# Kernel tuning notes

Measured on AMD Instinct MI355X. Metric: run time of the kernel, lower is better.

Reference implementation:

```python
import jax, jax.numpy as jnp
import numpy as np

B, T, HID = 2, 512, 1024
H, D, K = 16, 64, 4          # heads, head_dim, short-conv kernel
P = H * D                    # projection_dim
E, TOPK, I, IS = 8, 2, 768, 768  # experts, top_k, expert inter, shared inter
EPS = 1e-5


def setup_inputs() -> dict:
    key = jax.random.key(0)
    ks = jax.random.split(key, 24)
    def r(i, shape, s=0.02):
        return jax.random.normal(ks[i], shape, jnp.float32) * s
    return {
        "x": jax.random.normal(ks[0], (B, T, HID), jnp.float32),
        "norm1_w": jnp.ones((HID,), jnp.float32),
        "wq": r(1, (HID, P)), "wk": r(2, (HID, P)), "wv": r(3, (HID, P)),
        "cq": r(4, (P, K), 0.5), "ck": r(5, (P, K), 0.5), "cv": r(6, (P, K), 0.5),
        "fa": r(7, (HID, D)), "fb": r(8, (D, P)), "bp": r(9, (HID, H)),
        "ga": r(10, (HID, D)), "gb": r(11, (D, P)),
        "A_log": jnp.log(jax.random.uniform(ks[12], (H, 1), jnp.float32, 1.0, 16.0)),
        "dt_bias": r(13, (H, D), 0.1),
        "onorm_w": jnp.ones((D,), jnp.float32),
        "wo": r(14, (P, HID)),
        "norm2_w": jnp.ones((HID,), jnp.float32),
        "gate_w": r(15, (HID, E)), "gate_b": r(16, (E,), 0.1),
        "wg_e": r(17, (E, HID, I)), "wu_e": r(18, (E, HID, I)), "wd_e": r(19, (E, I, HID)),
        "wg_s": r(20, (HID, IS)), "wu_s": r(21, (HID, IS)), "wd_s": r(22, (IS, HID)),
    }


def _rms(x, w, eps=EPS):
    return x * jax.lax.rsqrt(jnp.mean(x * x, axis=-1, keepdims=True) + eps) * w


def _dwconv_silu(x, w):
    # causal depthwise conv, NLC layout: out[b,t,c] = sum_k w[c,k] * x[b, t-(K-1)+k, c]
    xp = jnp.pad(x, ((0, 0), (K - 1, 0), (0, 0)))
    out = sum(w[:, k] * xp[:, k:k + x.shape[1], :] for k in range(K))
    return jax.nn.silu(out)


def _delta_attn(x, wq, wk, wv, cq, ck, cv, fa, fb, bp, ga, gb, A_log, dt_bias, onorm_w, wo):
    q = _dwconv_silu(x @ wq, cq).reshape(B, T, H, D)
    k = _dwconv_silu(x @ wk, ck).reshape(B, T, H, D)
    v = _dwconv_silu(x @ wv, cv).reshape(B, T, H, D)
    # L2-style rms normalization of q/k (no weight, eps=1e-6), then asymmetric scaling
    q = q * jax.lax.rsqrt(jnp.mean(q * q, -1, keepdims=True) + 1e-6)
    k = k * jax.lax.rsqrt(jnp.mean(k * k, -1, keepdims=True) + 1e-6)
    scale = float(D) ** -0.5
    q = (scale ** 2) * q
    k = scale * k
    # fine-grained per-channel gated decay + per-head write strength
    a = ((x @ fa) @ fb).reshape(B, T, H, D)
    g = jnp.exp(-jnp.exp(A_log)[None, None] * jax.nn.softplus(a + dt_bias))  # (B,T,H,D)
    beta = jax.nn.sigmoid(x @ bp)  # (B,T,H)

    def step(S, qkvgb):
        qt, kt, vt, gt, bt = qkvgb            # (B,H,D) each, bt (B,H)
        S = S * gt[..., None]                  # decay over key dim, S: (B,H,Dk,Dv)
        pred = jnp.einsum('bhk,bhkv->bhv', kt, S)
        S = S + jnp.einsum('bhk,bhv->bhkv', kt, (vt - pred) * bt[..., None])
        o = jnp.einsum('bhk,bhkv->bhv', qt, S)
        return S, o

    xs = tuple(jnp.moveaxis(t_, 1, 0) for t_ in (q, k, v, g, beta))
    S0 = jnp.zeros((B, H, D, D), x.dtype)
    _, o = jax.lax.scan(step, S0, xs)
    o = jnp.moveaxis(o, 0, 1)                  # (B,T,H,D)
    gate = ((x @ ga) @ gb).reshape(B, T, H, D)
    o = _rms(o, onorm_w) * jax.nn.sigmoid(gate)
    return o.reshape(B, T, P) @ wo


def _moe(x, gate_w, gate_b, wg_e, wu_e, wd_e, wg_s, wu_s, wd_s):
    n = x.reshape(-1, HID)                     # (N, HID)
    scores = jax.nn.sigmoid(n @ gate_w)        # sigmoid router
    biased = scores + gate_b                   # e_score_correction bias (selection only)
    _, inds = jax.lax.top_k(biased, TOPK)      # n_group==1 -> plain top-k
    w = jnp.take_along_axis(scores, inds, -1)  # gather ORIGINAL scores
    w = w / (w.sum(-1, keepdims=True) + 1e-20) # renormalize; routed_scaling=1.0
    N = n.shape[0]
    comb = jnp.zeros((N, E), n.dtype).at[jnp.arange(N)[:, None], inds].add(w)
    hg = jnp.einsum('nd,edi->eni', n, wg_e)
    hu = jnp.einsum('nd,edi->eni', n, wu_e)
    eo = jnp.einsum('eni,eih->enh', jax.nn.silu(hg) * hu, wd_e)
    routed = jnp.einsum('ne,enh->nh', comb, eo)
    shared = (jax.nn.silu(n @ wg_s) * (n @ wu_s)) @ wd_s
    return (routed + shared).reshape(x.shape)


def _forward(x, norm1_w, wq, wk, wv, cq, ck, cv, fa, fb, bp, ga, gb, A_log, dt_bias,
             onorm_w, wo, norm2_w, gate_w, gate_b, wg_e, wu_e, wd_e, wg_s, wu_s, wd_s):
    h = x + _delta_attn(_rms(x, norm1_w), wq, wk, wv, cq, ck, cv, fa, fb, bp, ga, gb,
                        A_log, dt_bias, onorm_w, wo)
    return h + _moe(_rms(h, norm2_w), gate_w, gate_b, wg_e, wu_e, wd_e, wg_s, wu_s, wd_s)


def reference(x, norm1_w, wq, wk, wv, cq, ck, cv, fa, fb, bp, ga, gb, A_log, dt_bias,
              onorm_w, wo, norm2_w, gate_w, gate_b, wg_e, wu_e, wd_e, wg_s, wu_s, wd_s):
    return _forward(x, norm1_w, wq, wk, wv, cq, ck, cv, fa, fb, bp, ga, gb, A_log,
                    dt_bias, onorm_w, wo, norm2_w, gate_w, gate_b, wg_e, wu_e, wd_e,
                    wg_s, wu_s, wd_s)
```

## Files before the change

### kernel.cpp

```cpp
#include <hip/hip_runtime.h>
#include <hip/hip_bf16.h>
#include <math.h>

#define Bb 2
#define Tt 512
#define HIDD 1024
#define Hh 16
#define Dd 64
#define Pp 1024
#define Kc 4
#define Ee 8
#define Ii 768
#define ISs 768
#define Ntok (Bb*Tt)
#define NASSIGN (2*Ntok)
#define NPAD 2112
#define CH 16
#define NCH (Tt/CH)

typedef __attribute__((ext_vector_type(8))) short bf16x8;
typedef __attribute__((ext_vector_type(4))) float floatx4;

__device__ __forceinline__ float sigmoidf_(float x){ return 1.f/(1.f+expf(-x)); }
__device__ __forceinline__ float siluf_(float x){ return x/(1.f+expf(-x)); }
__device__ __forceinline__ float bf2f(__hip_bfloat16 b){ return __bfloat162float(b); }

__device__ __forceinline__ void async16(void* lds, const void* g) {
  __builtin_amdgcn_global_load_lds(
      (const __attribute__((address_space(1))) void*)g,
      (__attribute__((address_space(3))) void*)lds, 16, 0, 0);
}

template<int CTRL>
__device__ __forceinline__ float dpp_add(float x){
  int y = __builtin_amdgcn_update_dpp(0, __float_as_int(x), CTRL, 0xF, 0xF, true);
  return x + __int_as_float(y);
}

__global__ void rms_split_kernel(const float* __restrict__ x, const float* __restrict__ w,
                                 __hip_bfloat16* __restrict__ hi, __hip_bfloat16* __restrict__ lo,
                                 float eps) {
  int row = blockIdx.x;
  const float* xr = x + (size_t)row*HIDD;
  float s = 0.f;
  for (int i = threadIdx.x; i < HIDD; i += 256){ float v = xr[i]; s += v*v; }
  #pragma unroll
  for (int off=32; off; off>>=1) s += __shfl_down(s, off, 64);
  __shared__ float red[4];
  if ((threadIdx.x & 63)==0) red[threadIdx.x>>6] = s;
  __syncthreads();
  float tot = red[0]+red[1]+red[2]+red[3];
  float sc = rsqrtf(tot/(float)HIDD + eps);
  for (int i = threadIdx.x; i < HIDD; i += 256) {
    float v = xr[i]*sc*w[i];
    __hip_bfloat16 h = __float2bfloat16(v);
    hi[(size_t)row*HIDD+i] = h;
    lo[(size_t)row*HIDD+i] = __float2bfloat16(v - bf2f(h));
  }
}

__global__ void trans_split4_kernel(const float* __restrict__ wq, const float* __restrict__ wk,
                                    const float* __restrict__ wv, const float* __restrict__ wo,
                                    __hip_bfloat16* __restrict__ qkv_hi, __hip_bfloat16* __restrict__ qkv_lo,
                                    __hip_bfloat16* __restrict__ wo_hi, __hip_bfloat16* __restrict__ wo_lo) {
  int z = blockIdx.z;
  const float* src = (z==0)?wq:(z==1)?wk:(z==2)?wv:wo;
  __hip_bfloat16* hi = (z<3) ? qkv_hi + (size_t)z*Pp*HIDD : wo_hi;
  __hip_bfloat16* lo = (z<3) ? qkv_lo + (size_t)z*Pp*HIDD : wo_lo;
  __shared__ float tile[32][33];
  int n0 = blockIdx.x*32, k0 = blockIdx.y*32;
  int tx = threadIdx.x & 31, ty0 = threadIdx.x >> 5;
  #pragma unroll
  for (int j=0;j<4;j++){ int ty = ty0 + j*8; tile[ty][tx] = src[(size_t)(k0+ty)*1024 + n0+tx]; }
  __syncthreads();
  #pragma unroll
  for (int j=0;j<4;j++){
    int ty = ty0 + j*8;
    float v = tile[tx][ty];
    __hip_bfloat16 h = __float2bfloat16(v);
    hi[(size_t)(n0+ty)*1024 + k0+tx] = h;
    lo[(size_t)(n0+ty)*1024 + k0+tx] = __float2bfloat16(v - bf2f(h));
  }
}

__global__ void trans_kernel(const float* __restrict__ src, __hip_bfloat16* __restrict__ dst,
                             int K, int N, long sbs, long dbs) {
  src += (size_t)blockIdx.z * sbs; dst += (size_t)blockIdx.z * dbs;
  __shared__ float tile[32][33];
  int n0 = blockIdx.x*32, k0 = blockIdx.y*32;
  int tx = threadIdx.x & 31, ty0 = threadIdx.x >> 5;
  #pragma unroll
  for (int j=0;j<4;j++){ int ty = ty0 + j*8; tile[ty][tx] = src[(size_t)(k0+ty)*N + n0+tx]; }
  __syncthreads();
  #pragma unroll
  for (int j=0;j<4;j++){ int ty = ty0 + j*8; dst[(size_t)(n0+ty)*K + k0+tx] = __float2bfloat16(tile[tx][ty]); }
}

__global__ void trans_pair_kernel(const float* __restrict__ a, const float* __restrict__ b2,
                                  __hip_bfloat16* __restrict__ da, __hip_bfloat16* __restrict__ db,
                                  int K, int N) {
  const float* src = blockIdx.z ? b2 : a;
  __hip_bfloat16* dst = blockIdx.z ? db : da;
  __shared__ float tile[32][33];
  int n0 = blockIdx.x*32, k0 = blockIdx.y*32;
  int tx = threadIdx.x & 31, ty0 = threadIdx.x >> 5;
  #pragma unroll
  for (int j=0;j<4;j++){ int ty = ty0 + j*8; tile[ty][tx] = src[(size_t)(k0+ty)*N + n0+tx]; }
  __syncthreads();
  #pragma unroll
  for (int j=0;j<4;j++){ int ty = ty0 + j*8; dst[(size_t)(n0+ty)*K + k0+tx] = __float2bfloat16(tile[tx][ty]); }
}

__global__ void trans_inter_kernel(const float* __restrict__ sa, const float* __restrict__ sb2,
                                   __hip_bfloat16* __restrict__ dst, int K, int N,
                                   long sbs, long dbs) {
  int e = blockIdx.z >> 1, phase = blockIdx.z & 1;
  const float* src = (phase ? sb2 : sa) + (size_t)e*sbs;
  dst += (size_t)e*dbs;
  __shared__ float tile[32][33];
  int n0 = blockIdx.x*32, k0 = blockIdx.y*32;
  int tx = threadIdx.x & 31, ty0 = threadIdx.x >> 5;
  #pragma unroll
  for (int j=0;j<4;j++){ int ty = ty0 + j*8; tile[ty][tx] = src[(size_t)(k0+ty)*N + n0+tx]; }
  __syncthreads();
  #pragma unroll
  for (int j=0;j<4;j++){
    int ty = ty0 + j*8;
    dst[(size_t)(2*(n0+ty)+phase)*K + k0+tx] = __float2bfloat16(tile[tx][ty]);
  }
}

__device__ __forceinline__ int lds_off(int row, int slot){
  return row*128 + (((slot ^ row)&7)<<4);
}

template<int MODE, int ACC>
__global__ __launch_bounds__(256)
void gemm_k(const __hip_bfloat16* __restrict__ A, const __hip_bfloat16* __restrict__ BT,
            void* __restrict__ C, int M, int N, int K, int lda, const float* __restrict__ resid,
            const int* __restrict__ counts, const int* __restrict__ prefix,
            const int* __restrict__ ctok, const int* __restrict__ cslot,
            const float* __restrict__ cwt) {
  int Me = M;
  int moff = 0;
  if (MODE == 3 || MODE == 4 || MODE == 6) {
    int e = blockIdx.z;
    Me = counts[e]; moff = prefix[e];
    A  += (size_t)moff * lda;
    BT += (size_t)e * (size_t)N * K;
  }
  int row0 = blockIdx.y * 64;
  if (row0 >= Me) return;
  int col0 = blockIdx.x * 64;

  __shared__ __attribute__((aligned(16))) short As[64*64];
  __shared__ __attribute__((aligned(16))) short Bs[64*64];
  const int lane = threadIdx.x & 63;
  const int w    = threadIdx.x >> 6;
  const int wr = w >> 1, wc = w & 1;
  const int srow = lane >> 3;
  const int sch  = (lane & 7) ^ (srow & 7);
  const int q = lane >> 4, r16 = lane & 15;

  const __hip_bfloat16* Ag = A  + (size_t)row0 * lda;
  const __hip_bfloat16* Bg = BT + (size_t)col0 * K;

  floatx4 acc[2][2] = {};

  for (int k0 = 0; k0 < K; k0 += 64) {
    #pragma unroll
    for (int ii = 0; ii < 2; ++ii) {
      const int inst = w + ii*4;
      const int r = inst*8 + srow;
      async16((char*)As + inst*1024, Ag + (size_t)r*lda + (size_t)(k0 + sch*8));
      async16((char*)Bs + inst*1024, Bg + (size_t)r*K   + (size_t)(k0 + sch*8));
    }
    __syncthreads();
    #pragma unroll
    for (int kk = 0; kk < 2; ++kk) {
      int slot = kk*4 + q;
      bf16x8 a0 = *(const bf16x8*)((const char*)As + lds_off(wr*32 +      r16, slot));
      bf16x8 a1 = *(const bf16x8*)((const char*)As + lds_off(wr*32 + 16 + r16, slot));
      bf16x8 b0 = *(const bf16x8*)((const char*)Bs + lds_off(wc*32 +      r16, slot));
      bf16x8 b1 = *(const bf16x8*)((const char*)Bs + lds_off(wc*32 + 16 + r16, slot));
      acc[0][0] = __builtin_amdgcn_mfma_f32_16x16x32_bf16(a0, b0, acc[0][0], 0, 0, 0);
      acc[0][1] = __builtin_amdgcn_mfma_f32_16x16x32_bf16(a0, b1, acc[0][1], 0, 0, 0);
      acc[1][0] = __builtin_amdgcn_mfma_f32_16x16x32_bf16(a1, b0, acc[1][0], 0, 0, 0);
      acc[1][1] = __builtin_amdgcn_mfma_f32_16x16x32_bf16(a1, b1, acc[1][1], 0, 0, 0);
    }
    __syncthreads();
  }

  #pragma unroll
  for (int mi = 0; mi < 2; ++mi) {
    #pragma unroll
    for (int r = 0; r < 4; ++r) {
      int grow = row0 + wr*32 + mi*16 + q*4 + r;
      if (grow >= Me) continue;
      #pragma unroll
      for (int ni = 0; ni < 2; ++ni) {
        int gcol = col0 + wc*32 + ni*16 + r16;
        float v = acc[mi][ni][r];
        if (MODE == 0) {
          float* Cp = (float*)C + (size_t)grow*N + gcol;
          if (ACC) v += *Cp;
          *Cp = v;
        } else if (MODE == 2) {
          float* Cp = (float*)C + (size_t)grow*N + gcol;
          if (ACC) v += *Cp;
          *Cp = v + resid[(size_t)grow*N + gcol];
        } else if (MODE == 1) {
          ((__hip_bfloat16*)C)[(size_t)grow*N + gcol] = __float2bfloat16(v);
        } else if (MODE == 3) {
          ((__hip_bfloat16*)C)[(size_t)(moff+grow)*N + gcol] = __float2bfloat16(v);
        } else if (MODE == 4) {
          int rc = moff + grow;
          int tok = ctok[rc], sl = cslot[rc];
          ((__hip_bfloat16*)C)[((size_t)tok*2 + sl)*N + gcol] = __float2bfloat16(cwt[rc]*v);
        } else if (MODE == 5) {
          int hh2 = gcol >> 6, d2 = gcol & 63;
          float t2 = v + cwt[hh2*64 + d2];
          float sp = (t2 > 20.f) ? t2 : log1pf(expf(t2));
          ((float*)C)[(size_t)grow*N + gcol] = expf(-expf(resid[hh2]) * sp);
        } else {
          float pv = __shfl_xor(v, 1, 64);
          if ((lane & 1) == 0) {
            float rglu = siluf_(v) * pv;
            int pcol = gcol >> 1;
            size_t orow = (MODE == 6) ? (size_t)(moff + grow) : (size_t)grow;
            ((__hip_bfloat16*)C)[orow*(N/2) + pcol] = __float2bfloat16(rglu);
          }
        }
      }
    }
  }
}

template<int MODE>
__global__ __launch_bounds__(256)
void gemm3_k(const __hip_bfloat16* __restrict__ Ahi, const __hip_bfloat16* __restrict__ Alo,
             const __hip_bfloat16* __restrict__ Bhi, const __hip_bfloat16* __restrict__ Blo,
             float* __restrict__ C, int M, int N, int K, const float* __restrict__ resid) {
  int row0 = blockIdx.y * 64;
  int col0 = blockIdx.x * 64;

  __shared__ __attribute__((aligned(16))) short As[64*64];
  __shared__ __attribute__((aligned(16))) short Bs[64*64];
  const int lane = threadIdx.x & 63;
  const int w    = threadIdx.x >> 6;
  const int wr = w >> 1, wc = w & 1;
  const int srow = lane >> 3;
  const int sch  = (lane & 7) ^ (srow & 7);
  const int q = lane >> 4, r16 = lane & 15;

  floatx4 acc[2][2] = {};

  for (int p = 0; p < 3; ++p) {
    const __hip_bfloat16* Ag = ((p==2)? Alo : Ahi) + (size_t)row0 * K;
    const __hip_bfloat16* Bg = ((p==1)? Blo : Bhi) + (size_t)col0 * K;
    for (int k0 = 0; k0 < K; k0 += 64) {
      #pragma unroll
      for (int ii = 0; ii < 2; ++ii) {
        const int inst = w + ii*4;
        const int r = inst*8 + srow;
        async16((char*)As + inst*1024, Ag + (size_t)r*K + (size_t)(k0 + sch*8));
        async16((char*)Bs + inst*1024, Bg + (size_t)r*K + (size_t)(k0 + sch*8));
      }
      __syncthreads();
      #pragma unroll
      for (int kk = 0; kk < 2; ++kk) {
        int slot = kk*4 + q;
        bf16x8 a0 = *(const bf16x8*)((const char*)As + lds_off(wr*32 +      r16, slot));
        bf16x8 a1 = *(const bf16x8*)((const char*)As + lds_off(wr*32 + 16 + r16, slot));
        bf16x8 b0 = *(const bf16x8*)((const char*)Bs + lds_off(wc*32 +      r16, slot));
        bf16x8 b1 = *(const bf16x8*)((const char*)Bs + lds_off(wc*32 + 16 + r16, slot));
        acc[0][0] = __builtin_amdgcn_mfma_f32_16x16x32_bf16(a0, b0, acc[0][0], 0, 0, 0);
        acc[0][1] = __builtin_amdgcn_mfma_f32_16x16x32_bf16(a0, b1, acc[0][1], 0, 0, 0);
        acc[1][0] = __builtin_amdgcn_mfma_f32_16x16x32_bf16(a1, b0, acc[1][0], 0, 0, 0);
        acc[1][1] = __builtin_amdgcn_mfma_f32_16x16x32_bf16(a1, b1, acc[1][1], 0, 0, 0);
      }
      __syncthreads();
    }
  }

  #pragma unroll
  for (int mi = 0; mi < 2; ++mi) {
    #pragma unroll
    for (int r = 0; r < 4; ++r) {
      int grow = row0 + wr*32 + mi*16 + q*4 + r;
      #pragma unroll
      for (int ni = 0; ni < 2; ++ni) {
        int gcol = col0 + wc*32 + ni*16 + r16;
        float v = acc[mi][ni][r];
        if (MODE == 2) v += resid[(size_t)grow*N + gcol];
        C[(size_t)grow*N + gcol] = v;
      }
    }
  }
}

__global__ void conv_norm_kernel(const float* __restrict__ in,
                                 const float* __restrict__ cq, const float* __restrict__ ck,
                                 const float* __restrict__ cv,
                                 float* __restrict__ qc, float* __restrict__ kc,
                                 float* __restrict__ vc) {
  int tok = blockIdx.x;
  int mode = blockIdx.y;
  const float* w = (mode==0) ? cq : (mode==1) ? ck : cv;
  float* outp    = (mode==0) ? qc : (mode==1) ? kc : vc;
  int colOff = mode << 10;
  int t = threadIdx.x;
  int c0 = t*4;
  int tloc = tok & (Tt-1);

  float wv[4][4];
  #pragma unroll
  for (int i=0;i<4;i++){
    float4 w4 = ((const float4*)w)[c0+i];
    wv[i][0]=w4.x; wv[i][1]=w4.y; wv[i][2]=w4.z; wv[i][3]=w4.w;
  }
  float acc[4] = {0.f,0.f,0.f,0.f};
  #pragma unroll
  for (int j=0;j<Kc;j++){
    int tt = tloc - (Kc-1) + j;
    if (tt >= 0){
      float4 xv = *(const float4*)&in[(size_t)(tok-(Kc-1)+j)*3072 + colOff + c0];
      acc[0] += wv[0][j]*xv.x;
      acc[1] += wv[1][j]*xv.y;
      acc[2] += wv[2][j]*xv.z;
      acc[3] += wv[3][j]*xv.w;
    }
  }
  float val[4];
  #pragma unroll
  for (int i=0;i<4;i++) val[i] = siluf_(acc[i]);
  float scale = 1.f;
  if (mode < 2) {
    float ss = val[0]*val[0]+val[1]*val[1]+val[2]*val[2]+val[3]*val[3];
    ss += __shfl_xor(ss, 1, 64);
    ss += __shfl_xor(ss, 2, 64);
    ss += __shfl_xor(ss, 4, 64);
    ss += __shfl_xor(ss, 8, 64);
    scale = rsqrtf(ss/(float)Dd + 1e-6f) * ((mode==0) ? (1.f/64.f) : 0.125f);
  }
  float4 o4 = make_float4(val[0]*scale, val[1]*scale, val[2]*scale, val[3]*scale);
  *(float4*)&outp[(size_t)tok*Pp + c0] = o4;
}

__global__ void beta_kernel(const __hip_bfloat16* __restrict__ xn, const float* __restrict__ bp,
                            float* __restrict__ betab) {
  int row = blockIdx.x;
  int t = threadIdx.x;
  int n = t & 15, ch = t >> 4;
  float s = 0.f;
  for (int k = ch*64; k < ch*64+64; ++k)
    s += bf2f(xn[(size_t)row*HIDD + k]) * bp[k*16 + n];
  __shared__ float red[256];
  red[t] = s; __syncthreads();
  if (t < 16) {
    float tot = 0.f;
    #pragma unroll
    for (int c2 = 0; c2 < 16; ++c2) tot += red[c2*16 + t];
    betab[(size_t)row*16 + t] = sigmoidf_(tot);
  }
}

__global__ void moe_rms_scores_kernel(const float* __restrict__ h, const float* __restrict__ w2,
                                      const float* __restrict__ gw,
                                      __hip_bfloat16* __restrict__ hn, float* __restrict__ scores) {
  int row = blockIdx.x;
  const float* hr = h + (size_t)row*HIDD;
  float s = 0.f;
  for (int i = threadIdx.x; i < HIDD; i += 256){ float v = hr[i]; s += v*v; }
  #pragma unroll
  for (int off=32; off; off>>=1) s += __shfl_down(s, off, 64);
  __shared__ float red[4];
  if ((threadIdx.x & 63)==0) red[threadIdx.x>>6] = s;
  __syncthreads();
  float sc = rsqrtf((red[0]+red[1]+red[2]+red[3])/(float)HIDD + 1e-5f);
  float acc[Ee] = {};
  for (int i = threadIdx.x; i < HIDD; i += 256){
    float xv = hr[i]*sc*w2[i];
    hn[(size_t)row*HIDD + i] = __float2bfloat16(xv);
    #pragma unroll
    for (int e=0;e<Ee;e++) acc[e] += xv*gw[i*Ee+e];
  }
  #pragma unroll
  for (int e=0;e<Ee;e++){
    #pragma unroll
    for (int off=32; off; off>>=1) acc[e] += __shfl_down(acc[e], off, 64);
  }
  __shared__ float red2[4][Ee];
  if ((threadIdx.x & 63)==0){
    #pragma unroll
    for (int e=0;e<Ee;e++) red2[threadIdx.x>>6][e] = acc[e];
  }
  __syncthreads();
  if (threadIdx.x < Ee)
    scores[(size_t)row*Ee + threadIdx.x] =
      red2[0][threadIdx.x]+red2[1][threadIdx.x]+red2[2][threadIdx.x]+red2[3][threadIdx.x];
}

__global__ __launch_bounds__(64)
void scan_kernel(const float* __restrict__ q, const float* __restrict__ k,
                 const float* __restrict__ v, const float* __restrict__ g,
                 const float* __restrict__ beta, float* __restrict__ o) {
  const int vb = blockIdx.x & 15;
  const int hh = (blockIdx.x >> 4) & 15;
  const int b  = blockIdx.x >> 8;
  const int lane = threadIdx.x;
  const int kq = lane & 15;
  const int vi = lane >> 4;
  const int v0 = vb*4;
  const int rb = b*Tt;

  __shared__ __attribute__((aligned(16))) float sq[2][CH][64];
  __shared__ __attribute__((aligned(16))) float sk[2][CH][64];
  __shared__ __attribute__((aligned(16))) float sg[2][CH][64];
  __shared__ __attribute__((aligned(16))) float sbv[Tt][4];
  __shared__ float sb[Tt];

  #pragma unroll
  for (int i=0;i<Tt/64;i++)
    async16(&sbv[i*64][0], v + (size_t)(rb + i*64 + lane)*Pp + hh*64 + v0);
  #pragma unroll
  for (int i=0;i<Tt/64;i++)
    sb[i*64+lane] = beta[(size_t)(rb + i*64 + lane)*Hh + hh];

  auto stage = [&](int t0, int pb) {
    const int srow = lane >> 4, sch4 = (lane & 15)*4;
    #pragma unroll
    for (int ii=0; ii<4; ++ii) {
      size_t gbase = (size_t)(rb + t0 + ii*4 + srow)*Pp + hh*64;
      async16(&sq[pb][ii*4][0], q + gbase + sch4);
      async16(&sk[pb][ii*4][0], k + gbase + sch4);
      async16(&sg[pb][ii*4][0], g + gbase + sch4);
    }
  };

  float S0=0.f, S1=0.f, S2=0.f, S3=0.f;

  stage(0, 0);
  asm volatile("s_waitcnt vmcnt(0)" ::: "memory");

  for (int c=0; c<NCH; ++c) {
    int pb = c & 1;
    if (c+1 < NCH) {
      stage((c+1)*CH, pb^1);
      asm volatile("s_waitcnt vmcnt(12)" ::: "memory");
    } else {
      asm volatile("s_waitcnt vmcnt(0)" ::: "memory");
    }
    __builtin_amdgcn_sched_barrier(0);
    #pragma unroll
    for (int i=0;i<CH;i++){
      int t = c*CH + i;
      float4 k4 = *(const float4*)&sk[pb][i][kq*4];
      float4 g4 = *(const float4*)&sg[pb][i][kq*4];
      float4 q4 = *(const float4*)&sq[pb][i][kq*4];
      float vv = sbv[t][vi];
      float bt = sb[t];
      S0 *= g4.x; S1 *= g4.y; S2 *= g4.z; S3 *= g4.w;
      float pred = S0*k4.x + S1*k4.y + S2*k4.z + S3*k4.w;
      pred = dpp_add<0xB1>(pred);
      pred = dpp_add<0x4E>(pred);
      pred = dpp_add<0x141>(pred);
      pred = dpp_add<0x140>(pred);
      float upd = (vv - pred) * bt;
      S0 += k4.x*upd; S1 += k4.y*upd; S2 += k4.z*upd; S3 += k4.w*upd;
      float acc = S0*q4.x + S1*q4.y + S2*q4.z + S3*q4.w;
      acc = dpp_add<0xB1>(acc);
      acc = dpp_add<0x4E>(acc);
      acc = dpp_add<0x141>(acc);
      acc = dpp_add<0x140>(acc);
      if (kq == 0) o[(size_t)(rb+t)*Pp + hh*64 + v0 + vi] = acc;
    }
  }
}

__global__ void onorm_gate_split_kernel(const float* __restrict__ o, const float* __restrict__ w,
                                        const float* __restrict__ gate,
                                        __hip_bfloat16* __restrict__ hi, __hip_bfloat16* __restrict__ lo) {
  int row = blockIdx.x*4 + (threadIdx.x>>6);
  int lane = threadIdx.x & 63;
  size_t idx = (size_t)row*Dd + lane;
  float v = o[idx];
  float s = v*v;
  #pragma unroll
  for (int off=32; off; off>>=1) s += __shfl_xor(s, off, 64);
  float r = v * rsqrtf(s/(float)Dd + 1e-5f) * w[lane] * sigmoidf_(gate[idx]);
  __hip_bfloat16 h = __float2bfloat16(r);
  hi[idx] = h;
  lo[idx] = __float2bfloat16(r - bf2f(h));
}

__global__ void router_kernel(const float* __restrict__ logits, const float* __restrict__ gate_b,
                              int* __restrict__ counts, int* __restrict__ tok_list,
                              int* __restrict__ slot_list, float* __restrict__ wt_list) {
  int n = blockIdx.x*256 + threadIdx.x;
  if (n >= Ntok) return;
  float sc[Ee], bi[Ee];
  #pragma unroll
  for (int e=0;e<Ee;e++){ float s = sigmoidf_(logits[n*Ee+e]); sc[e]=s; bi[e]=s+gate_b[e]; }
  int i0=0;
  #pragma unroll
  for (int e=1;e<Ee;e++) if (bi[e] > bi[i0]) i0=e;
  int i1=-1;
  #pragma unroll
  for (int e=0;e<Ee;e++){ if (e==i0) continue; if (i1<0 || bi[e] > bi[i1]) i1=e; }
  float w0=sc[i0], w1=sc[i1];
  float inv = 1.f/(w0+w1+1e-20f);
  w0*=inv; w1*=inv;
  int p0 = atomicAdd(&counts[i0],1);
  tok_list[i0*Ntok+p0]=n; slot_list[i0*Ntok+p0]=0; wt_list[i0*Ntok+p0]=w0;
  int p1 = atomicAdd(&counts[i1],1);
  tok_list[i1*Ntok+p1]=n; slot_list[i1*Ntok+p1]=1; wt_list[i1*Ntok+p1]=w1;
}

__global__ void prefix_kernel(const int* __restrict__ counts, int* __restrict__ prefix) {
  if (threadIdx.x==0 && blockIdx.x==0){ int s=0; for (int e=0;e<Ee;e++){ prefix[e]=s; s+=counts[e]; } }
}

__global__ void compact_kernel(const int* __restrict__ counts, const int* __restrict__ prefix,
                               const int* __restrict__ tok_list, const int* __restrict__ slot_list,
                               const float* __restrict__ wt_list,
                               int* __restrict__ ctok, int* __restrict__ cslot, float* __restrict__ cwt) {
  int e = blockIdx.x; int c = counts[e], p = prefix[e];
  for (int i = threadIdx.x; i < c; i += 256) {
    ctok[p+i]  = tok_list[e*Ntok+i];
    cslot[p+i] = slot_list[e*Ntok+i];
    cwt[p+i]   = wt_list[e*Ntok+i];
  }
}

__global__ void gather_kernel(const __hip_bfloat16* __restrict__ hn, const int* __restrict__ ctok,
                              __hip_bfloat16* __restrict__ Ae) {
  int r = blockIdx.x;
  int t = threadIdx.x;
  ((int4*)(Ae + (size_t)r*HIDD))[t] = ((const int4*)(hn + (size_t)ctok[r]*HIDD))[t];
}

__global__ void final_kernel(const float* __restrict__ h, const __hip_bfloat16* __restrict__ routed,
                             const float* __restrict__ shr, float* __restrict__ out) {
  int idx = blockIdx.x*256 + threadIdx.x;
  if (idx >= Ntok*HIDD) return;
  int n = idx >> 10, c = idx & 1023;
  out[idx] = h[idx] + bf2f(routed[(size_t)n*2*HIDD + c]) + bf2f(routed[(size_t)n*2*HIDD + HIDD + c]) + shr[idx];
}

extern "C" void kernel_launch(void* const* d_in, const int* in_sizes, int n_in,
                              void* d_out, int out_size, void* d_ws, size_t ws_size,
                              hipStream_t stream) {
  (void)in_sizes; (void)n_in; (void)out_size; (void)ws_size;
  const float* x        = (const float*)d_in[0];
  const float* norm1_w  = (const float*)d_in[1];
  const float* wq       = (const float*)d_in[2];
  const float* wk       = (const float*)d_in[3];
  const float* wv       = (const float*)d_in[4];
  const float* cq       = (const float*)d_in[5];
  const float* ck       = (const float*)d_in[6];
  const float* cv       = (const float*)d_in[7];
  const float* fa       = (const float*)d_in[8];
  const float* fb       = (const float*)d_in[9];
  const float* bp       = (const float*)d_in[10];
  const float* ga       = (const float*)d_in[11];
  const float* gb       = (const float*)d_in[12];
  const float* A_log    = (const float*)d_in[13];
  const float* dt_bias  = (const float*)d_in[14];
  const float* onorm_w  = (const float*)d_in[15];
  const float* wo       = (const float*)d_in[16];
  const float* norm2_w  = (const float*)d_in[17];
  const float* gate_w   = (const float*)d_in[18];
  const float* gate_b   = (const float*)d_in[19];
  const float* wg_e     = (const float*)d_in[20];
  const float* wu_e     = (const float*)d_in[21];
  const float* wd_e     = (const float*)d_in[22];
  const float* wg_s     = (const float*)d_in[23];
  const float* wu_s     = (const float*)d_in[24];
  const float* wd_s     = (const float*)d_in[25];
  float* out = (float*)d_out;

  char* base = (char*)d_ws;
  size_t off = 0;
  auto alloc = [&](size_t bytes)->char* {
    off = (off + 255) & ~(size_t)255;
    char* p = base + off; off += bytes; return p;
  };
  float* hbuf = (float*)alloc((size_t)Ntok*HIDD*4);
  size_t uStart = (off + 255) & ~(size_t)255;

  off = uStart;
  __hip_bfloat16* xn      = (__hip_bfloat16*)alloc((size_t)Ntok*HIDD*2);
  __hip_bfloat16* xn_lo   = (__hip_bfloat16*)alloc((size_t)Ntok*HIDD*2);
  __hip_bfloat16* wqkv_t  = (__hip_bfloat16*)alloc((size_t)3*Pp*HIDD*2);
  __hip_bfloat16* wqkv_lo = (__hip_bfloat16*)alloc((size_t)3*Pp*HIDD*2);
  float*          qkvlin  = (float*)alloc((size_t)Ntok*3*Pp*4);
  float*          qc      = (float*)alloc((size_t)Ntok*Pp*4);
  float*          kc      = (float*)alloc((size_t)Ntok*Pp*4);
  float*          vc      = (float*)alloc((size_t)Ntok*Pp*4);
  float*          gbuf    = (float*)alloc((size_t)Ntok*Pp*4);
  float*          gatebuf = (float*)alloc((size_t)Ntok*Pp*4);
  float*          obuf    = (float*)alloc((size_t)Ntok*Pp*4);
  __hip_bfloat16* atmp12  = (__hip_bfloat16*)alloc((size_t)Ntok*2*Dd*2);
  float*          betab   = (float*)alloc((size_t)Ntok*Hh*4);
  __hip_bfloat16* obuf_hi = (__hip_bfloat16*)alloc((size_t)Ntok*Pp*2);
  __hip_bfloat16* obuf_lo = (__hip_bfloat16*)alloc((size_t)Ntok*Pp*2);
  __hip_bfloat16* wo_t    = (__hip_bfloat16*)alloc((size_t)HIDD*Pp*2);
  __hip_bfloat16* wo_lo   = (__hip_bfloat16*)alloc((size_t)HIDD*Pp*2);
  __hip_bfloat16* fg_t    = (__hip_bfloat16*)alloc((size_t)2*Dd*HIDD*2);
  __hip_bfloat16* fb_t    = (__hip_bfloat16*)alloc((size_t)Pp*Dd*2);
  __hip_bfloat16* gb_t    = (__hip_bfloat16*)alloc((size_t)Pp*Dd*2);

  off = uStart;
  __hip_bfloat16* hn      = (__hip_bfloat16*)alloc((size_t)Ntok*HIDD*2);
  float*          scores  = (float*)alloc((size_t)Ntok*Ee*4);
  int*            counts  = (int*)alloc(64);
  int*            prefix  = (int*)alloc(64);
  int*            tok_list  = (int*)alloc((size_t)Ee*Ntok*4);
  int*            slot_list = (int*)alloc((size_t)Ee*Ntok*4);
  float*          wt_list   = (float*)alloc((size_t)Ee*Ntok*4);
  int*            ctok    = (int*)alloc((size_t)NPAD*4);
  int*            cslot   = (int*)alloc((size_t)NPAD*4);
  float*          cwt     = (float*)alloc((size_t)NPAD*4);
  __hip_bfloat16* egu_t   = (__hip_bfloat16*)alloc((size_t)Ee*2*Ii*HIDD*2);
  __hip_bfloat16* sgu_t   = (__hip_bfloat16*)alloc((size_t)2*ISs*HIDD*2);
  __hip_bfloat16* sd_t    = (__hip_bfloat16*)alloc((size_t)HIDD*ISs*2);
  __hip_bfloat16* act     = (__hip_bfloat16*)alloc((size_t)NPAD*Ii*2);
  __hip_bfloat16* sgb     = (__hip_bfloat16*)alloc((size_t)Ntok*ISs*2);
  __hip_bfloat16* routed  = (__hip_bfloat16*)alloc((size_t)Ntok*2*HIDD*2);
  float*          shout   = (float*)alloc((size_t)Ntok*HIDD*4);
  __hip_bfloat16* Ae      = (__hip_bfloat16*)alloc((size_t)NPAD*HIDD*2);
  __hip_bfloat16* ed_t    = (__hip_bfloat16*)alloc((size_t)Ee*HIDD*Ii*2);

  dim3 blk(256);
  #define NO5 nullptr, nullptr, nullptr, nullptr, nullptr

  rms_split_kernel<<<Ntok, blk, 0, stream>>>(x, norm1_w, xn, xn_lo, 1e-5f);
  trans_split4_kernel<<<dim3(32,32,4), blk, 0, stream>>>(wq, wk, wv, wo,
                                                         wqkv_t, wqkv_lo, wo_t, wo_lo);
  trans_pair_kernel<<<dim3(2,32,2), blk, 0, stream>>>(fa, ga, fg_t, fg_t + (size_t)Dd*HIDD, HIDD, Dd);
  trans_pair_kernel<<<dim3(32,2,2), blk, 0, stream>>>(fb, gb, fb_t, gb_t, Dd, Pp);

  gemm3_k<0><<<dim3(48,16,1), blk, 0, stream>>>(xn, xn_lo, wqkv_t, wqkv_lo, qkvlin,
                                                Ntok, 3*Pp, HIDD, nullptr);
  conv_norm_kernel<<<dim3(Ntok,3,1), blk, 0, stream>>>(qkvlin, cq, ck, cv, qc, kc, vc);
  gemm_k<1,0><<<dim3(2,16,1), blk, 0, stream>>>(xn, fg_t, atmp12, Ntok, 2*Dd, HIDD, HIDD, NO5, nullptr);
  gemm_k<5,0><<<dim3(16,16,1), blk, 0, stream>>>(atmp12, fb_t, gbuf, Ntok, Pp, Dd, 2*Dd,
                                                 A_log, nullptr, nullptr, nullptr, nullptr, dt_bias);
  gemm_k<0,0><<<dim3(16,16,1), blk, 0, stream>>>(atmp12+Dd, gb_t, gatebuf, Ntok, Pp, Dd, 2*Dd, NO5, nullptr);
  beta_kernel<<<Ntok, blk, 0, stream>>>(xn, bp, betab);
  scan_kernel<<<Bb*Hh*16, dim3(64), 0, stream>>>(qc, kc, vc, gbuf, betab, obuf);
  onorm_gate_split_kernel<<<(Ntok*Hh)/4, blk, 0, stream>>>(obuf, onorm_w, gatebuf, obuf_hi, obuf_lo);
  gemm3_k<2><<<dim3(16,16,1), blk, 0, stream>>>(obuf_hi, obuf_lo, wo_t, wo_lo, hbuf,
                                                Ntok, HIDD, Pp, x);

  moe_rms_scores_kernel<<<Ntok, blk, 0, stream>>>(hbuf, norm2_w, gate_w, hn, scores);
  hipMemsetAsync(counts, 0, Ee*sizeof(int), stream);
  router_kernel<<<(Ntok+255)/256, blk, 0, stream>>>(scores, gate_b, counts, tok_list, slot_list, wt_list);
  prefix_kernel<<<1, 64, 0, stream>>>(counts, prefix);
  compact_kernel<<<Ee, blk, 0, stream>>>(counts, prefix, tok_list, slot_list, wt_list, ctok, cslot, cwt);
  gather_kernel<<<NASSIGN, dim3(128), 0, stream>>>(hn, ctok, Ae);
  trans_inter_kernel<<<dim3(24,32,2*Ee), blk, 0, stream>>>(wg_e, wu_e, egu_t,
      HIDD, Ii, (long)HIDD*Ii, (long)2*Ii*HIDD);
  gemm_k<6,0><<<dim3(24,16,Ee), blk, 0, stream>>>(Ae, egu_t, act, Ntok, 2*Ii, HIDD, HIDD,
                                                  nullptr, counts, prefix, nullptr, nullptr, nullptr);
  trans_kernel<<<dim3(32,24,Ee), blk, 0, stream>>>(wd_e, ed_t,
      Ii, HIDD, (long)Ii*HIDD, (long)HIDD*Ii);
  gemm_k<4,0><<<dim3(16,16,Ee), blk, 0, stream>>>(act, ed_t, routed, Ntok, HIDD, Ii, Ii,
                                                  nullptr, counts, prefix, ctok, cslot, cwt);
  trans_inter_kernel<<<dim3(24,32,2), blk, 0, stream>>>(wg_s, wu_s, sgu_t, HIDD, ISs, 0, 0);
  trans_kernel<<<dim3(32,24,1), blk, 0, stream>>>(wd_s, sd_t, ISs, HIDD, 0, 0);
  gemm_k<7,0><<<dim3(24,16,1), blk, 0, stream>>>(hn, sgu_t, sgb, Ntok, 2*ISs, HIDD, HIDD, NO5, nullptr);
  gemm_k<0,0><<<dim3(16,16,1), blk, 0, stream>>>(sgb, sd_t, shout, Ntok, HIDD, ISs, ISs, NO5, nullptr);

  final_kernel<<<(Ntok*HIDD+255)/256, blk, 0, stream>>>(hbuf, routed, shout, out);
}
```

Measured before the change: 356.7 us.

## Software-pipeline delta scan with register double-buffering and LDS-staged output

The recurrent scan kernel now uses a triple-buffered LDS ring with 8-step chunks. The next chunk's operands are prefetched into registers with inline ds_read instructions while the current chunk computes, so LDS latency sits off the serial dependency chain. Per-step scalar global stores of the output are replaced by writes into an LDS buffer, followed by one coalesced float4 store pass at the end. The cost is much higher register pressure from two register operand sets, plus extra LDS, and hand-written waitcnt counts that must match the number of async loads.

```diff
diff --git a/kernel.cpp b/kernel.cpp
--- a/kernel.cpp
+++ b/kernel.cpp
@@ -15,8 +15,8 @@
 #define Ntok (Bb*Tt)
 #define NASSIGN (2*Ntok)
 #define NPAD 2112
-#define CH 16
-#define NCH (Tt/CH)
+#define SCH 8
+#define SNCH (Tt/SCH)
 
 typedef __attribute__((ext_vector_type(8))) short bf16x8;
 typedef __attribute__((ext_vector_type(4))) float floatx4;
@@ -35,6 +35,17 @@
 __device__ __forceinline__ float dpp_add(float x){
   int y = __builtin_amdgcn_update_dpp(0, __float_as_int(x), CTRL, 0xF, 0xF, true);
   return x + __int_as_float(y);
+}
+
+__device__ __forceinline__ void ds_read128(floatx4& d, const float* p){
+  asm volatile("ds_read_b128 %0, %1"
+    : "=v"(d)
+    : "v"((const __attribute__((address_space(3))) float*)p));
+}
+__device__ __forceinline__ void ds_read32f(float& d, const float* p){
+  asm volatile("ds_read_b32 %0, %1"
+    : "=v"(d)
+    : "v"((const __attribute__((address_space(3))) float*)p));
 }
 
 __global__ void rms_split_kernel(const float* __restrict__ x, const float* __restrict__ w,
@@ -401,6 +412,46 @@
       red2[0][threadIdx.x]+red2[1][threadIdx.x]+red2[2][threadIdx.x]+red2[3][threadIdx.x];
 }
 
+#define REGLOAD(bufi, tbase, K,G,Q,VV,BT) do { \
+  const int _b = (bufi); const int _t0 = (tbase); \
+  _Pragma("unroll") \
+  for (int _i=0;_i<SCH;_i++){ \
+    ds_read128(K[_i], &sk[_b][_i][kq*4]); \
+    ds_read128(G[_i], &sg[_b][_i][kq*4]); \
+    ds_read128(Q[_i], &sq[_b][_i][kq*4]); \
+    ds_read32f(VV[_i], &sbv[_t0+_i][vi]); \
+    ds_read32f(BT[_i], &sb[_t0+_i]); \
+  } \
+} while(0)
+
+#define SSTEP(K,G,Q,VV,BT,_i,_t) do { \
+  floatx4 k4=K[_i], g4=G[_i], q4=Q[_i]; \
+  float vvv=VV[_i], bt=BT[_i]; \
+  S0*=g4.x; S1*=g4.y; S2*=g4.z; S3*=g4.w; \
+  float pred = S0*k4.x + S1*k4.y + S2*k4.z + S3*k4.w; \
+  pred = dpp_add<0xB1>(pred); pred = dpp_add<0x4E>(pred); \
+  pred = dpp_add<0x141>(pred); pred = dpp_add<0x140>(pred); \
+  float upd = (vvv - pred) * bt; \
+  S0 += k4.x*upd; S1 += k4.y*upd; S2 += k4.z*upd; S3 += k4.w*upd; \
+  float acc = S0*q4.x + S1*q4.y + S2*q4.z + S3*q4.w; \
+  acc = dpp_add<0xB1>(acc); acc = dpp_add<0x4E>(acc); \
+  acc = dpp_add<0x141>(acc); acc = dpp_add<0x140>(acc); \
+  if (kq == 0) so[_t][vi] = acc; \
+} while(0)
+
+#define SITER(c, KC,GC,QC,VC,BC, KN,GN,QN,VN,BN) do { \
+  if ((c)+1 < SNCH) { \
+    if ((c)+2 < SNCH) asm volatile("s_waitcnt vmcnt(6)" ::: "memory"); \
+    else              asm volatile("s_waitcnt vmcnt(0)" ::: "memory"); \
+    REGLOAD(((c)+1)%3, ((c)+1)*SCH, KN,GN,QN,VN,BN); \
+    if ((c)+3 < SNCH) stage(((c)+3)*SCH, ((c)+3)%3); \
+  } \
+  _Pragma("unroll") \
+  for (int _s=0;_s<SCH;_s++) SSTEP(KC,GC,QC,VC,BC,_s,(c)*SCH+_s); \
+  asm volatile("s_waitcnt lgkmcnt(0)" ::: "memory"); \
+  __builtin_amdgcn_sched_barrier(0); \
+} while(0)
+
 __global__ __launch_bounds__(64)
 void scan_kernel(const float* __restrict__ q, const float* __restrict__ k,
                  const float* __restrict__ v, const float* __restrict__ g,
@@ -414,67 +465,54 @@
   const int v0 = vb*4;
   const int rb = b*Tt;
 
-  __shared__ __attribute__((aligned(16))) float sq[2][CH][64];
-  __shared__ __attribute__((aligned(16))) float sk[2][CH][64];
-  __shared__ __attribute__((aligned(16))) float sg[2][CH][64];
+  __shared__ __attribute__((aligned(16))) float sq[3][SCH][64];
+  __shared__ __attribute__((aligned(16))) float sk[3][SCH][64];
+  __shared__ __attribute__((aligned(16))) float sg[3][SCH][64];
   __shared__ __attribute__((aligned(16))) float sbv[Tt][4];
   __shared__ float sb[Tt];
+  __shared__ __attribute__((aligned(16))) float so[Tt][4];
+
+  #pragma unroll
+  for (int i=0;i<Tt/64;i++)
+    sb[i*64+lane] = beta[(size_t)(rb + i*64 + lane)*Hh + hh];
+  asm volatile("s_waitcnt vmcnt(0)" ::: "memory");
 
   #pragma unroll
   for (int i=0;i<Tt/64;i++)
     async16(&sbv[i*64][0], v + (size_t)(rb + i*64 + lane)*Pp + hh*64 + v0);
-  #pragma unroll
-  for (int i=0;i<Tt/64;i++)
-    sb[i*64+lane] = beta[(size_t)(rb + i*64 + lane)*Hh + hh];
-
-  auto stage = [&](int t0, int pb) {
+
+  auto stage = [&](int t0, int buf) {
     const int srow = lane >> 4, sch4 = (lane & 15)*4;
     #pragma unroll
-    for (int ii=0; ii<4; ++ii) {
+    for (int ii=0; ii<2; ++ii) {
       size_t gbase = (size_t)(rb + t0 + ii*4 + srow)*Pp + hh*64;
-      async16(&sq[pb][ii*4][0], q + gbase + sch4);
-      async16(&sk[pb][ii*4][0], k + gbase + sch4);
-      async16(&sg[pb][ii*4][0], g + gbase + sch4);
+      async16(&sq[buf][ii*4][0], q + gbase + sch4);
+      async16(&sk[buf][ii*4][0], k + gbase + sch4);
+      async16(&sg[buf][ii*4][0], g + gbase + sch4);
     }
   };
 
-  float S0=0.f, S1=0.f, S2=0.f, S3=0.f;
+  floatx4 Ka[SCH],Ga[SCH],Qa[SCH], Kb[SCH],Gb[SCH],Qb[SCH];
+  float Va[SCH],Bta[SCH], Vb2[SCH],Btb[SCH];
+  float S0=0.f,S1=0.f,S2=0.f,S3=0.f;
 
   stage(0, 0);
-  asm volatile("s_waitcnt vmcnt(0)" ::: "memory");
-
-  for (int c=0; c<NCH; ++c) {
-    int pb = c & 1;
-    if (c+1 < NCH) {
-      stage((c+1)*CH, pb^1);
-      asm volatile("s_waitcnt vmcnt(12)" ::: "memory");
-    } else {
-      asm volatile("s_waitcnt vmcnt(0)" ::: "memory");
-    }
-    __builtin_amdgcn_sched_barrier(0);
-    #pragma unroll
-    for (int i=0;i<CH;i++){
-      int t = c*CH + i;
-      float4 k4 = *(const float4*)&sk[pb][i][kq*4];
-      float4 g4 = *(const float4*)&sg[pb][i][kq*4];
-      float4 q4 = *(const float4*)&sq[pb][i][kq*4];
-      float vv = sbv[t][vi];
-      float bt = sb[t];
-      S0 *= g4.x; S1 *= g4.y; S2 *= g4.z; S3 *= g4.w;
-      float pred = S0*k4.x + S1*k4.y + S2*k4.z + S3*k4.w;
-      pred = dpp_add<0xB1>(pred);
-      pred = dpp_add<0x4E>(pred);
-      pred = dpp_add<0x141>(pred);
-      pred = dpp_add<0x140>(pred);
-      float upd = (vv - pred) * bt;
-      S0 += k4.x*upd; S1 += k4.y*upd; S2 += k4.z*upd; S3 += k4.w*upd;
-      float acc = S0*q4.x + S1*q4.y + S2*q4.z + S3*q4.w;
-      acc = dpp_add<0xB1>(acc);
-      acc = dpp_add<0x4E>(acc);
-      acc = dpp_add<0x141>(acc);
-      acc = dpp_add<0x140>(acc);
-      if (kq == 0) o[(size_t)(rb+t)*Pp + hh*64 + v0 + vi] = acc;
-    }
+  stage(SCH, 1);
+  asm volatile("s_waitcnt vmcnt(6)" ::: "memory");
+  REGLOAD(0, 0, Ka,Ga,Qa,Va,Bta);
+  stage(2*SCH, 2);
+  asm volatile("s_waitcnt lgkmcnt(0)" ::: "memory");
+  __builtin_amdgcn_sched_barrier(0);
+
+  for (int cp = 0; cp < SNCH; cp += 2) {
+    SITER(cp,   Ka,Ga,Qa,Va,Bta, Kb,Gb,Qb,Vb2,Btb);
+    SITER(cp+1, Kb,Gb,Qb,Vb2,Btb, Ka,Ga,Qa,Va,Bta);
+  }
+
+  #pragma unroll
+  for (int i=0;i<Tt/64;i++){
+    int t = i*64 + lane;
+    *(float4*)&o[(size_t)(rb+t)*Pp + hh*64 + v0] = *(const float4*)&so[t][0];
   }
 }
 
```

After: 345.9 us. 3.0% less time.
